# Performance work log

Measured on AMD Instinct MI355X. Metric: run time of the kernel, lower is better.

## Reference

```python
import jax, jax.numpy as jnp
import numpy as np

B, S, HID = 2, 2048, 2048
H, D_NOPE, D_ROPE = 16, 128, 64
KV_LORA = 192            # forced so v_head dim == pad_hd == 128 (see torch view)
NUM_SLOTS, MAX_LEN = 8, 2048
SCALE = D_NOPE ** -0.5


def setup_inputs() -> dict:
    key = jax.random.key(0)
    ks = jax.random.split(key, 4)
    return {
        "hidden_states": jax.random.normal(ks[0], (B, S, HID), jnp.float32),
        "Wq": jax.random.normal(ks[1], (H * (D_NOPE + D_ROPE), HID), jnp.float32) * 0.02,
        "Wkv": jax.random.normal(ks[2], (KV_LORA + D_ROPE, HID), jnp.float32) * 0.02,
        "Wo": jax.random.normal(ks[3], (HID, H * D_NOPE), jnp.float32) * 0.02,
        "k_cache": jnp.zeros((NUM_SLOTS, MAX_LEN, 1, D_NOPE), jnp.float32),
        "v_cache": jnp.zeros((NUM_SLOTS, MAX_LEN, 1, D_NOPE), jnp.float32),
        "slot_mapping": jnp.arange(B, dtype=jnp.int32),
        "kv_start_indices": jnp.zeros((B,), jnp.int32),
        "seq_lens": jnp.full((B,), S, jnp.int32),
        "positions": jnp.arange(S, dtype=jnp.int32),
    }


def reference(hidden_states, Wq, Wkv, Wo, k_cache, v_cache,
              slot_mapping, kv_start_indices, seq_lens, positions):
    # q / low-rank kv projections (nn.Linear convention: x @ W.T)
    q = (hidden_states @ Wq.T).reshape(B, S, H, D_NOPE + D_ROPE)
    q_nope = q[..., :D_NOPE]                       # [B,S,H,128]
    kv = hidden_states @ Wkv.T                     # [B,S,256]
    k = kv[..., :D_NOPE][:, :, None, :]            # [B,S,1,128] single latent kv head
    v = kv[..., D_NOPE:][:, :, None, :]            # [B,S,1,128]

    # paged KV-cache scatter (prefill: kv_start_indices == 0, write [0:S))
    k_cache = k_cache.at[slot_mapping, :S].set(k)
    v_cache = v_cache.at[slot_mapping, :S].set(v)

    # gather history back (max_l = seq_lens.max() == S at prefill, static)
    k_hist = k_cache[slot_mapping, :S]             # [B,L,1,128]
    v_hist = v_cache[slot_mapping, :S]

    # MQA attention: sum over singleton kv-head axis == repeat_interleave broadcast
    scores = jnp.einsum('bshd,blod->bhsl', q_nope, k_hist) * SCALE  # [B,H,S,L]
    causal = jnp.triu(jnp.ones((S, S), bool), k=1)  # diagonal = start(0)+1
    scores = jnp.where(causal[None, None], -jnp.inf, scores)
    attn = jax.nn.softmax(scores, axis=-1)
    out = jnp.einsum('bhsl,blod->bshd', attn, v_hist)  # [B,S,H,128]
    out = out.reshape(B, S, H * D_NOPE)
    return out @ Wo.T
```

## Files before the change

kernel.cpp:

```cpp
#include <hip/hip_runtime.h>
#include <hip/hip_bf16.h>
#include <stdint.h>


typedef __attribute__((ext_vector_type(4))) float f32x4;
typedef __attribute__((ext_vector_type(8))) short bf16x8;
typedef __attribute__((ext_vector_type(4))) short bf16x4;

__device__ __forceinline__ unsigned short f2bf(float f) {
    union { float f; unsigned u; } v; v.f = f;
    unsigned u = v.u;
    return (unsigned short)((u + 0x7fffu + ((u >> 16) & 1u)) >> 16);
}

__device__ __forceinline__ short bf_rn(float f) {
    __hip_bfloat16 h = __float2bfloat16(f);
    short s; __builtin_memcpy(&s, &h, 2); return s;
}

__device__ __forceinline__ float exp2_raw(float x) {
#if __has_builtin(__builtin_amdgcn_exp2f)
    return __builtin_amdgcn_exp2f(x);
#else
    return exp2f(x);
#endif
}

#define MFMA32(a,b,c) __builtin_amdgcn_mfma_f32_16x16x32_bf16((a),(b),(c),0,0,0)
#if defined(__HIP_DEVICE_COMPILE__)
#define MFMA16(a,b,c) __builtin_amdgcn_mfma_f32_16x16x16bf16_1k((a),(b),(c),0,0,0)
#else
#define MFMA16(a,b,c) (c)
#endif

#define GLD_LDS16(g,l) __builtin_amdgcn_global_load_lds( \
    (const __attribute__((address_space(1))) unsigned int*)(g), \
    (__attribute__((address_space(3))) unsigned int*)(l), 16, 0, 0)

__global__ void cvt_all(const float* __restrict__ in, unsigned short* __restrict__ out, int n4) {
    const int stride = gridDim.x * blockDim.x;
    for (int i = blockIdx.x * blockDim.x + threadIdx.x; i < n4; i += stride) {
        float4 v = ((const float4*)in)[i];
        ushort4 r;
        r.x = f2bf(v.x); r.y = f2bf(v.y); r.z = f2bf(v.z); r.w = f2bf(v.w);
        ((ushort4*)out)[i] = r;
    }
}

__global__ void cvt_wqkv(const float* __restrict__ wq, const float* __restrict__ wkv,
                         unsigned short* __restrict__ out) {
    const int row = blockIdx.x;
    const bool isq = (row < 2048);
    const float sc = isq ? 0.1275174331181861f : 1.0f;
    const float* srcp = isq ? (wq + (long)((row >> 7) * 192 + (row & 127)) * 2048)
                            : (wkv + (long)(row - 2048) * 2048);
    const float4* ip = (const float4*)srcp;
    ushort4* op = (ushort4*)(out + (long)row * 2048);
    for (int i = threadIdx.x; i < 512; i += 256) {
        float4 v = ip[i];
        ushort4 r;
        r.x = f2bf(v.x * sc); r.y = f2bf(v.y * sc);
        r.z = f2bf(v.z * sc); r.w = f2bf(v.w * sc);
        op[i] = r;
    }
}

__global__ void transpose_v(const unsigned short* __restrict__ qkv, unsigned short* __restrict__ vt) {
    __shared__ unsigned short tile[32][33];
    const int b = blockIdx.z, dt = blockIdx.y, st = blockIdx.x;
    const int x = threadIdx.x, y = threadIdx.y;
    const int s0 = st * 32, d0 = dt * 32;
    #pragma unroll
    for (int i = 0; i < 4; ++i)
        tile[y + i * 8][x] = qkv[((long)(b * 2048 + s0 + y + i * 8)) * 2304 + 2176 + d0 + x];
    __syncthreads();
    #pragma unroll
    for (int i = 0; i < 4; ++i)
        vt[((long)(b * 128 + d0 + y + i * 8)) * 2048 + s0 + x] = tile[x][y + i * 8];
}

template<int OUT_BF16>
__global__ __launch_bounds__(256, 2)
void gemm_bt(const unsigned short* __restrict__ A,
             const unsigned short* __restrict__ B,
             void* __restrict__ Cp, int M, int N, int K) {
    __shared__ unsigned short As[2][128 * 64];
    __shared__ unsigned short Bs[2][128 * 64];
    const int t = threadIdx.x;
    const int wave = t >> 6, lane = t & 63;
    const int wr = wave >> 1, wc = wave & 1;
    const int l15 = lane & 15, l4 = lane >> 4;

    const int nbx = gridDim.x;
    const int nwg = nbx * gridDim.y;
    const int borig = blockIdx.y * nbx + blockIdx.x;
    const int bswz = (borig & 7) * (nwg >> 3) + (borig >> 3);
    const long m0 = (bswz / nbx) * 128L, n0 = (bswz % nbx) * 128L;

    const unsigned short* asrc[4];
    const unsigned short* bsrc[4];
    #pragma unroll
    for (int it = 0; it < 4; ++it) {
        const int c = it * 4 + wave;
        const int row = c * 8 + (lane >> 3);
        const int gsw = (lane & 7) ^ (row & 7);
        asrc[it] = A + (m0 + row) * K + gsw * 8;
        bsrc[it] = B + (n0 + row) * K + gsw * 8;
    }

#define GSTAGE(bufi, kt) do { \
    _Pragma("unroll") \
    for (int it = 0; it < 4; ++it) { \
        const int c = it * 4 + wave; \
        GLD_LDS16(asrc[it] + (kt) * 64, &As[bufi][c * 512]); \
        GLD_LDS16(bsrc[it] + (kt) * 64, &Bs[bufi][c * 512]); \
    } \
} while (0)

    f32x4 acc[4][4] = {};
    const int nk = K >> 6;
    GSTAGE(0, 0);
    int cur = 0;
    for (int kt = 0; kt < nk; ++kt) {
        __builtin_amdgcn_s_barrier();
        if (kt + 1 < nk) {
            GSTAGE(cur ^ 1, kt + 1);
            asm volatile("s_waitcnt vmcnt(8)" ::: "memory");
        } else {
            asm volatile("s_waitcnt vmcnt(0)" ::: "memory");
        }
        __builtin_amdgcn_s_barrier();

        const unsigned short* as = &As[cur][0];
        const unsigned short* bs = &Bs[cur][0];
        __builtin_amdgcn_s_setprio(1);
        #pragma unroll
        for (int ks = 0; ks < 2; ++ks) {
            bf16x8 af[4], bfr[4];
            #pragma unroll
            for (int m = 0; m < 4; ++m) {
                const int row = wr * 64 + m * 16 + l15;
                const int slot = (ks * 4 + l4) ^ (row & 7);
                af[m] = *(const bf16x8*)(as + row * 64 + slot * 8);
            }
            #pragma unroll
            for (int n = 0; n < 4; ++n) {
                const int row = wc * 64 + n * 16 + l15;
                const int slot = (ks * 4 + l4) ^ (row & 7);
                bfr[n] = *(const bf16x8*)(bs + row * 64 + slot * 8);
            }
            #pragma unroll
            for (int m = 0; m < 4; ++m)
                #pragma unroll
                for (int n = 0; n < 4; ++n)
                    acc[m][n] = MFMA32(af[m], bfr[n], acc[m][n]);
        }
        __builtin_amdgcn_s_setprio(0);
        cur ^= 1;
    }
#undef GSTAGE

    #pragma unroll
    for (int m = 0; m < 4; ++m)
        #pragma unroll
        for (int n = 0; n < 4; ++n) {
            const long rg = m0 + wr * 64 + m * 16 + l4 * 4;
            const long cg = n0 + wc * 64 + n * 16 + l15;
            #pragma unroll
            for (int i = 0; i < 4; ++i) {
                float v = acc[m][n][i];
                if (OUT_BF16) ((unsigned short*)Cp)[(rg + i) * N + cg] = f2bf(v);
                else          ((float*)Cp)[(rg + i) * N + cg] = v;
            }
        }
}

__global__ __launch_bounds__(256, 2)
void attn_fused(const unsigned short* __restrict__ QKV,
                const unsigned short* __restrict__ VT,
                unsigned short* __restrict__ AO) {
    __shared__ unsigned short Ks[2][64 * 128];
    __shared__ unsigned short Vs[2][128 * 64];
    const int t = threadIdx.x;
    const int wave = t >> 6, lane = t & 63;
    const int l15 = lane & 15, l4 = lane >> 4;
    const int bid = blockIdx.x;
    const int p = bid >> 4;
    const int hgb = bid & 15;
    const int hg = hgb >> 1, b = hgb & 1;
    const int h = hg * 2 + (wave >> 1);
    const int qsub = wave & 1;
    const long rowB = (long)b * 2048;

    const unsigned short* ksrc[4];
    const unsigned short* vsrc[4];
    #pragma unroll
    for (int it = 0; it < 4; ++it) {
        const int c = it * 4 + wave;
        const int krow = c * 4 + (lane >> 4);
        const int ksp = (lane & 15) ^ (krow & 15);
        ksrc[it] = QKV + (rowB + krow) * 2304 + 2048 + ksp * 8;
        const int vd = c * 8 + (lane >> 3);
        const int vsp = (lane & 7) ^ (vd & 7);
        vsrc[it] = VT + ((long)b * 128 + vd) * 2048 + vsp * 8;
    }

#define STAGE(bufi, jj0) do { \
    _Pragma("unroll") \
    for (int it = 0; it < 4; ++it) { \
        const int c = it * 4 + wave; \
        GLD_LDS16(ksrc[it] + (long)(jj0) * 2304, &Ks[bufi][c * 512]); \
        GLD_LDS16(vsrc[it] + (jj0), &Vs[bufi][c * 512]); \
    } \
} while (0)

    for (int ph = 0; ph < 2; ++ph) {
        const int qt = ph ? p : (63 - p);
        const int q0 = qt * 32;
        const int q0w = q0 + qsub * 16;
        const int nt = (qt >> 1) + 1;

        bf16x8 qf[4];
        {
            const unsigned short* qp = QKV + (rowB + q0w + l15) * 2304 + h * 128;
            #pragma unroll
            for (int kb = 0; kb < 4; ++kb)
                qf[kb] = *(const bf16x8*)(qp + kb * 32 + l4 * 8);
        }

        f32x4 o[8] = {};
        float lsum = 0.f;

        STAGE(0, 0);
        int cur = 0;

        for (int tt = 0; tt < nt; ++tt) {
            const int j0 = tt * 64;
            asm volatile("s_waitcnt vmcnt(0)" ::: "memory");
            __builtin_amdgcn_s_barrier();
            if (tt + 1 < nt) STAGE(cur ^ 1, j0 + 64);

            const unsigned short* ksBase = cur ? &Ks[1][0] : &Ks[0][0];
            f32x4 st[4];
            __builtin_amdgcn_s_setprio(1);
            #pragma unroll
            for (int jkv = 0; jkv < 4; ++jkv) {
                const unsigned short* krp = ksBase + (jkv * 16 + l15) * 128;
                f32x4 s0 = {};
                #pragma unroll
                for (int kb = 0; kb < 4; ++kb) {
                    const int slot = (kb * 4 + l4) ^ l15;
                    bf16x8 kf = *(const bf16x8*)(krp + slot * 8);
                    s0 = MFMA32(kf, qf[kb], s0);
                }
                st[jkv] = s0;
            }
            __builtin_amdgcn_s_setprio(0);

            if (tt + 1 == nt) {
                const int qrow = q0w + l15;
                #pragma unroll
                for (int jkv = 0; jkv < 4; ++jkv)
                    #pragma unroll
                    for (int i = 0; i < 4; ++i) {
                        const int kpos = j0 + jkv * 16 + l4 * 4 + i;
                        if (kpos > qrow) st[jkv][i] = -3.0e38f;
                    }
            }
            float ps = 0.f;
            bf16x4 pa[4];
            #pragma unroll
            for (int jkv = 0; jkv < 4; ++jkv) {
                float p0 = exp2_raw(st[jkv][0]);
                float p1 = exp2_raw(st[jkv][1]);
                float p2 = exp2_raw(st[jkv][2]);
                float p3 = exp2_raw(st[jkv][3]);
                ps += (p0 + p1) + (p2 + p3);
#if defined(__HIP_DEVICE_COMPILE__)
                unsigned r0, r1;
                asm("v_cvt_pk_bf16_f32 %0, %1, %2" : "=v"(r0) : "v"(p0), "v"(p1));
                asm("v_cvt_pk_bf16_f32 %0, %1, %2" : "=v"(r1) : "v"(p2), "v"(p3));
                union { unsigned u[2]; bf16x4 v; } cvt;
                cvt.u[0] = r0; cvt.u[1] = r1;
                pa[jkv] = cvt.v;
#else
                bf16x4 v = { bf_rn(p0), bf_rn(p1), bf_rn(p2), bf_rn(p3) };
                pa[jkv] = v;
#endif
            }
            lsum += ps;

            const unsigned short* vsBase = cur ? &Vs[1][0] : &Vs[0][0];
            __builtin_amdgcn_s_setprio(1);
            #pragma unroll
            for (int dj = 0; dj < 8; ++dj) {
                const int d = dj * 16 + l15;
                const unsigned short* vrow = vsBase + d * 64;
                const int dsw = (d & 7) << 3;
                #pragma unroll
                for (int jkv = 0; jkv < 4; ++jkv) {
                    bf16x4 vf = *(const bf16x4*)(vrow + ((jkv * 16 + l4 * 4) ^ dsw));
                    o[dj] = MFMA16(pa[jkv], vf, o[dj]);
                }
            }
            __builtin_amdgcn_s_setprio(0);
            cur ^= 1;
        }

        float lrow = lsum;
        lrow += __shfl_xor(lrow, 16);
        lrow += __shfl_xor(lrow, 32);
        float il[4];
        #pragma unroll
        for (int i = 0; i < 4; ++i)
            il[i] = 1.0f / __shfl(lrow, l4 * 4 + i);
        #pragma unroll
        for (int dj = 0; dj < 8; ++dj)
            #pragma unroll
            for (int i = 0; i < 4; ++i) {
                const long qrow = rowB + q0w + l4 * 4 + i;
                AO[qrow * 2048 + h * 128 + dj * 16 + l15] = (unsigned short)bf_rn(o[dj][i] * il[i]);
            }
        __syncthreads();
    }
#undef STAGE
}

extern "C" void kernel_launch(void* const* d_in, const int* in_sizes, int n_in,
                              void* d_out, int out_size, void* d_ws, size_t ws_size,
                              hipStream_t stream) {
    const float* hs  = (const float*)d_in[0];
    const float* Wq  = (const float*)d_in[1];
    const float* Wkv = (const float*)d_in[2];
    const float* Wo  = (const float*)d_in[3];
    char* ws = (char*)d_ws;
    unsigned short* h_bf   = (unsigned short*)(ws + 0);
    unsigned short* wqkv_bf= (unsigned short*)(ws + 16777216);
    unsigned short* wo_bf  = (unsigned short*)(ws + 26214400);
    unsigned short* qkv_bf = (unsigned short*)(ws + 34603008);
    unsigned short* vt_bf  = (unsigned short*)(ws + 53477376);
    unsigned short* ao_bf  = (unsigned short*)(ws + 54525952);
    float* out = (float*)d_out;

    cvt_all <<<2048, 256, 0, stream>>>(hs, h_bf, 2097152);
    cvt_all <<<2048, 256, 0, stream>>>(Wo, wo_bf, 1048576);
    cvt_wqkv<<<2304, 256, 0, stream>>>(Wq, Wkv, wqkv_bf);

    gemm_bt<1><<<dim3(18, 32), 256, 0, stream>>>(h_bf, wqkv_bf, qkv_bf, 4096, 2304, 2048);
    transpose_v<<<dim3(64, 4, 2), dim3(32, 8), 0, stream>>>(qkv_bf, vt_bf);
    attn_fused<<<dim3(512, 1, 1), 256, 0, stream>>>(qkv_bf, vt_bf, ao_bf);
    gemm_bt<0><<<dim3(16, 32), 256, 0, stream>>>(ao_bf, wo_bf, out, 4096, 2048, 2048);
}
```

Measured before the change: 188.5 us.

## Use 128x256 GEMM tiles with 8 waves and triple-buffered K=32 pipeline

```diff
diff --git a/kernel.cpp b/kernel.cpp
--- a/kernel.cpp
+++ b/kernel.cpp
@@ -80,83 +80,82 @@
 }
 
 template<int OUT_BF16>
-__global__ __launch_bounds__(256, 2)
+__global__ __launch_bounds__(512, 2)
 void gemm_bt(const unsigned short* __restrict__ A,
              const unsigned short* __restrict__ B,
              void* __restrict__ Cp, int M, int N, int K) {
-    __shared__ unsigned short As[2][128 * 64];
-    __shared__ unsigned short Bs[2][128 * 64];
+    __shared__ unsigned short As[3][128 * 32];
+    __shared__ unsigned short Bs[3][256 * 32];
     const int t = threadIdx.x;
     const int wave = t >> 6, lane = t & 63;
-    const int wr = wave >> 1, wc = wave & 1;
+    const int wr = wave >> 2, wc = wave & 3;
     const int l15 = lane & 15, l4 = lane >> 4;
 
     const int nbx = gridDim.x;
     const int nwg = nbx * gridDim.y;
     const int borig = blockIdx.y * nbx + blockIdx.x;
     const int bswz = (borig & 7) * (nwg >> 3) + (borig >> 3);
-    const long m0 = (bswz / nbx) * 128L, n0 = (bswz % nbx) * 128L;
-
-    const unsigned short* asrc[4];
-    const unsigned short* bsrc[4];
-    #pragma unroll
-    for (int it = 0; it < 4; ++it) {
-        const int c = it * 4 + wave;
-        const int row = c * 8 + (lane >> 3);
-        const int gsw = (lane & 7) ^ (row & 7);
-        asrc[it] = A + (m0 + row) * K + gsw * 8;
-        bsrc[it] = B + (n0 + row) * K + gsw * 8;
-    }
-
-#define GSTAGE(bufi, kt) do { \
-    _Pragma("unroll") \
-    for (int it = 0; it < 4; ++it) { \
-        const int c = it * 4 + wave; \
-        GLD_LDS16(asrc[it] + (kt) * 64, &As[bufi][c * 512]); \
-        GLD_LDS16(bsrc[it] + (kt) * 64, &Bs[bufi][c * 512]); \
-    } \
+    const long m0 = (bswz / nbx) * 128L;
+    const long n0 = (bswz % nbx) * 256L;
+
+    const int rowA = t >> 2;
+    const int sA = (t & 3) ^ ((rowA >> 1) & 3);
+    const unsigned short* aS = A + (m0 + rowA) * K + sA * 8;
+    const int rowB0 = t >> 2;
+    const int sB0 = (t & 3) ^ ((rowB0 >> 1) & 3);
+    const int g1 = t + 512;
+    const int rowB1 = g1 >> 2;
+    const int sB1 = (g1 & 3) ^ ((rowB1 >> 1) & 3);
+    const unsigned short* bS0 = B + (n0 + rowB0) * K + sB0 * 8;
+    const unsigned short* bS1 = B + (n0 + rowB1) * K + sB1 * 8;
+
+#define GSTAGE(bi, kt) do { \
+    GLD_LDS16(aS + (kt) * 32, &As[bi][wave * 512]); \
+    GLD_LDS16(bS0 + (kt) * 32, &Bs[bi][wave * 512]); \
+    GLD_LDS16(bS1 + (kt) * 32, &Bs[bi][4096 + wave * 512]); \
 } while (0)
 
     f32x4 acc[4][4] = {};
-    const int nk = K >> 6;
+    const int nk = K >> 5;
     GSTAGE(0, 0);
-    int cur = 0;
+    GSTAGE(1, 1);
+    int b0 = 0, b1 = 1, b2 = 2;
     for (int kt = 0; kt < nk; ++kt) {
-        __builtin_amdgcn_s_barrier();
-        if (kt + 1 < nk) {
-            GSTAGE(cur ^ 1, kt + 1);
-            asm volatile("s_waitcnt vmcnt(8)" ::: "memory");
+        if (kt + 2 < nk) {
+            GSTAGE(b2, kt + 2);
+            asm volatile("s_waitcnt vmcnt(6)" ::: "memory");
+        } else if (kt + 1 < nk) {
+            asm volatile("s_waitcnt vmcnt(3)" ::: "memory");
         } else {
             asm volatile("s_waitcnt vmcnt(0)" ::: "memory");
         }
         __builtin_amdgcn_s_barrier();
 
-        const unsigned short* as = &As[cur][0];
-        const unsigned short* bs = &Bs[cur][0];
+        const unsigned short* as = &As[0][0] + b0 * 4096;
+        const unsigned short* bs = &Bs[0][0] + b0 * 8192;
         __builtin_amdgcn_s_setprio(1);
-        #pragma unroll
-        for (int ks = 0; ks < 2; ++ks) {
-            bf16x8 af[4], bfr[4];
-            #pragma unroll
-            for (int m = 0; m < 4; ++m) {
-                const int row = wr * 64 + m * 16 + l15;
-                const int slot = (ks * 4 + l4) ^ (row & 7);
-                af[m] = *(const bf16x8*)(as + row * 64 + slot * 8);
-            }
-            #pragma unroll
-            for (int n = 0; n < 4; ++n) {
-                const int row = wc * 64 + n * 16 + l15;
-                const int slot = (ks * 4 + l4) ^ (row & 7);
-                bfr[n] = *(const bf16x8*)(bs + row * 64 + slot * 8);
-            }
-            #pragma unroll
-            for (int m = 0; m < 4; ++m)
-                #pragma unroll
-                for (int n = 0; n < 4; ++n)
-                    acc[m][n] = MFMA32(af[m], bfr[n], acc[m][n]);
-        }
+        bf16x8 af[4], bfr[4];
+        #pragma unroll
+        for (int m = 0; m < 4; ++m) {
+            const int row = wr * 64 + m * 16 + l15;
+            const int slot = l4 ^ ((row >> 1) & 3);
+            af[m] = *(const bf16x8*)(as + row * 32 + slot * 8);
+        }
+        #pragma unroll
+        for (int n = 0; n < 4; ++n) {
+            const int row = wc * 64 + n * 16 + l15;
+            const int slot = l4 ^ ((row >> 1) & 3);
+            bfr[n] = *(const bf16x8*)(bs + row * 32 + slot * 8);
+        }
+        #pragma unroll
+        for (int m = 0; m < 4; ++m)
+            #pragma unroll
+            for (int n = 0; n < 4; ++n)
+                acc[m][n] = MFMA32(af[m], bfr[n], acc[m][n]);
         __builtin_amdgcn_s_setprio(0);
-        cur ^= 1;
+        __builtin_amdgcn_s_barrier();
+
+        const int tmp = b0; b0 = b1; b1 = b2; b2 = tmp;
     }
 #undef GSTAGE
 
@@ -346,8 +345,8 @@
     cvt_all <<<2048, 256, 0, stream>>>(Wo, wo_bf, 1048576);
     cvt_wqkv<<<2304, 256, 0, stream>>>(Wq, Wkv, wqkv_bf);
 
-    gemm_bt<1><<<dim3(18, 32), 256, 0, stream>>>(h_bf, wqkv_bf, qkv_bf, 4096, 2304, 2048);
+    gemm_bt<1><<<dim3(9, 32), 512, 0, stream>>>(h_bf, wqkv_bf, qkv_bf, 4096, 2304, 2048);
     transpose_v<<<dim3(64, 4, 2), dim3(32, 8), 0, stream>>>(qkv_bf, vt_bf);
     attn_fused<<<dim3(512, 1, 1), 256, 0, stream>>>(qkv_bf, vt_bf, ao_bf);
-    gemm_bt<0><<<dim3(16, 32), 256, 0, stream>>>(ao_bf, wo_bf, out, 4096, 2048, 2048);
-}
+    gemm_bt<0><<<dim3(8, 32), 512, 0, stream>>>(ao_bf, wo_bf, out, 4096, 2048, 2048);
+}
```

After: 195.6 us. 1.04x slower.

## Load V fragments directly from global into registers instead of LDS staging

Applied to the files above, without the earlier changes.

```diff
diff --git a/kernel.cpp b/kernel.cpp
--- a/kernel.cpp
+++ b/kernel.cpp
@@ -180,7 +180,6 @@
                 const unsigned short* __restrict__ VT,
                 unsigned short* __restrict__ AO) {
     __shared__ unsigned short Ks[2][64 * 128];
-    __shared__ unsigned short Vs[2][128 * 64];
     const int t = threadIdx.x;
     const int wave = t >> 6, lane = t & 63;
     const int l15 = lane & 15, l4 = lane >> 4;
@@ -193,24 +192,20 @@
     const long rowB = (long)b * 2048;
 
     const unsigned short* ksrc[4];
-    const unsigned short* vsrc[4];
     #pragma unroll
     for (int it = 0; it < 4; ++it) {
         const int c = it * 4 + wave;
         const int krow = c * 4 + (lane >> 4);
         const int ksp = (lane & 15) ^ (krow & 15);
         ksrc[it] = QKV + (rowB + krow) * 2304 + 2048 + ksp * 8;
-        const int vd = c * 8 + (lane >> 3);
-        const int vsp = (lane & 7) ^ (vd & 7);
-        vsrc[it] = VT + ((long)b * 128 + vd) * 2048 + vsp * 8;
-    }
-
-#define STAGE(bufi, jj0) do { \
+    }
+    const unsigned short* vb = VT + ((long)b * 128 + l15) * 2048 + l4 * 4;
+
+#define STAGE_K(bufi, jj0) do { \
     _Pragma("unroll") \
     for (int it = 0; it < 4; ++it) { \
         const int c = it * 4 + wave; \
         GLD_LDS16(ksrc[it] + (long)(jj0) * 2304, &Ks[bufi][c * 512]); \
-        GLD_LDS16(vsrc[it] + (jj0), &Vs[bufi][c * 512]); \
     } \
 } while (0)
 
@@ -231,14 +226,25 @@
         f32x4 o[8] = {};
         float lsum = 0.f;
 
-        STAGE(0, 0);
+        STAGE_K(0, 0);
         int cur = 0;
 
         for (int tt = 0; tt < nt; ++tt) {
             const int j0 = tt * 64;
             asm volatile("s_waitcnt vmcnt(0)" ::: "memory");
             __builtin_amdgcn_s_barrier();
-            if (tt + 1 < nt) STAGE(cur ^ 1, j0 + 64);
+
+            bf16x4 vr[8][4];
+            {
+                const unsigned short* vbj = vb + j0;
+                #pragma unroll
+                for (int dj = 0; dj < 8; ++dj) {
+                    const bf16x4* vp = (const bf16x4*)(vbj + (long)dj * 32768);
+                    vr[dj][0] = vp[0];  vr[dj][1] = vp[4];
+                    vr[dj][2] = vp[8];  vr[dj][3] = vp[12];
+                }
+            }
+            if (tt + 1 < nt) STAGE_K(cur ^ 1, j0 + 64);
 
             const unsigned short* ksBase = cur ? &Ks[1][0] : &Ks[0][0];
             f32x4 st[4];
@@ -290,19 +296,12 @@
             }
             lsum += ps;
 
-            const unsigned short* vsBase = cur ? &Vs[1][0] : &Vs[0][0];
             __builtin_amdgcn_s_setprio(1);
             #pragma unroll
-            for (int dj = 0; dj < 8; ++dj) {
-                const int d = dj * 16 + l15;
-                const unsigned short* vrow = vsBase + d * 64;
-                const int dsw = (d & 7) << 3;
-                #pragma unroll
-                for (int jkv = 0; jkv < 4; ++jkv) {
-                    bf16x4 vf = *(const bf16x4*)(vrow + ((jkv * 16 + l4 * 4) ^ dsw));
-                    o[dj] = MFMA16(pa[jkv], vf, o[dj]);
-                }
-            }
+            for (int dj = 0; dj < 8; ++dj)
+                #pragma unroll
+                for (int jkv = 0; jkv < 4; ++jkv)
+                    o[dj] = MFMA16(pa[jkv], vr[dj][jkv], o[dj]);
             __builtin_amdgcn_s_setprio(0);
             cur ^= 1;
         }
@@ -323,7 +322,7 @@
             }
         __syncthreads();
     }
-#undef STAGE
+#undef STAGE_K
 }
 
 extern "C" void kernel_launch(void* const* d_in, const int* in_sizes, int n_in,
```

New measurement: 381.7 us. 102% more time.

## Replace double-buffered GEMM LDS pipeline with single-buffer synchronous loop

Applied to the files above, without the earlier changes.

```diff
diff --git a/kernel.cpp b/kernel.cpp
--- a/kernel.cpp
+++ b/kernel.cpp
@@ -84,8 +84,8 @@
 void gemm_bt(const unsigned short* __restrict__ A,
              const unsigned short* __restrict__ B,
              void* __restrict__ Cp, int M, int N, int K) {
-    __shared__ unsigned short As[2][128 * 64];
-    __shared__ unsigned short Bs[2][128 * 64];
+    __shared__ unsigned short As[128 * 64];
+    __shared__ unsigned short Bs[128 * 64];
     const int t = threadIdx.x;
     const int wave = t >> 6, lane = t & 63;
     const int wr = wave >> 1, wc = wave & 1;
@@ -108,31 +108,15 @@
         bsrc[it] = B + (n0 + row) * K + gsw * 8;
     }
 
-#define GSTAGE(bufi, kt) do { \
-    _Pragma("unroll") \
-    for (int it = 0; it < 4; ++it) { \
-        const int c = it * 4 + wave; \
-        GLD_LDS16(asrc[it] + (kt) * 64, &As[bufi][c * 512]); \
-        GLD_LDS16(bsrc[it] + (kt) * 64, &Bs[bufi][c * 512]); \
-    } \
-} while (0)
-
     f32x4 acc[4][4] = {};
-    const int nk = K >> 6;
-    GSTAGE(0, 0);
-    int cur = 0;
-    for (int kt = 0; kt < nk; ++kt) {
-        __builtin_amdgcn_s_barrier();
-        if (kt + 1 < nk) {
-            GSTAGE(cur ^ 1, kt + 1);
-            asm volatile("s_waitcnt vmcnt(8)" ::: "memory");
-        } else {
-            asm volatile("s_waitcnt vmcnt(0)" ::: "memory");
-        }
-        __builtin_amdgcn_s_barrier();
-
-        const unsigned short* as = &As[cur][0];
-        const unsigned short* bs = &Bs[cur][0];
+    for (int k0 = 0; k0 < K; k0 += 64) {
+        #pragma unroll
+        for (int it = 0; it < 4; ++it) {
+            const int c = it * 4 + wave;
+            GLD_LDS16(asrc[it] + k0, As + c * 512);
+            GLD_LDS16(bsrc[it] + k0, Bs + c * 512);
+        }
+        __syncthreads();
         __builtin_amdgcn_s_setprio(1);
         #pragma unroll
         for (int ks = 0; ks < 2; ++ks) {
@@ -141,13 +125,13 @@
             for (int m = 0; m < 4; ++m) {
                 const int row = wr * 64 + m * 16 + l15;
                 const int slot = (ks * 4 + l4) ^ (row & 7);
-                af[m] = *(const bf16x8*)(as + row * 64 + slot * 8);
+                af[m] = *(const bf16x8*)(As + row * 64 + slot * 8);
             }
             #pragma unroll
             for (int n = 0; n < 4; ++n) {
                 const int row = wc * 64 + n * 16 + l15;
                 const int slot = (ks * 4 + l4) ^ (row & 7);
-                bfr[n] = *(const bf16x8*)(bs + row * 64 + slot * 8);
+                bfr[n] = *(const bf16x8*)(Bs + row * 64 + slot * 8);
             }
             #pragma unroll
             for (int m = 0; m < 4; ++m)
@@ -156,9 +140,8 @@
                     acc[m][n] = MFMA32(af[m], bfr[n], acc[m][n]);
         }
         __builtin_amdgcn_s_setprio(0);
-        cur ^= 1;
-    }
-#undef GSTAGE
+        __syncthreads();
+    }
 
     #pragma unroll
     for (int m = 0; m < 4; ++m)
```

Measured after the change: 167.8 us. 1.12x faster.
